# Kernel tuning notes

Hardware: AMD Instinct MI355X
Metric: run time of the kernel (lower is better)

The kernel has to match this reference:

```python
import jax, jax.numpy as jnp
import numpy as np

B, L, D, Z, H, N, G = 8, 2048, 1024, 128, 2048, 16, 32
MAXPOS = 2048
EPS = 1e-5
PRIOR_COUNT = 2.0  # TimestepNorm prior pseudo-count


def setup_inputs() -> dict:
    ks = jax.random.split(jax.random.key(0), 12)
    std = 0.02  # bert init
    return {
        "x": jax.random.normal(ks[0], (B, L, D), jnp.float32),
        "prior_mean": jnp.zeros((G,), jnp.float32),
        "prior_logv": jnp.zeros((G,), jnp.float32),
        "tn_weight": jnp.ones((D,), jnp.float32),
        "tn_bias": jnp.zeros((D,), jnp.float32),
        "delta": jax.random.normal(ks[1], (D, N), jnp.float32),
        "alpha": jax.random.normal(ks[2], (D, N), jnp.float32),
        "ema_beta": jax.random.normal(ks[3], (D, N), jnp.float32),
        "ema_gamma": jax.random.normal(ks[4], (D, N), jnp.float32),
        "omega": jax.random.normal(ks[5], (D,), jnp.float32),
        "rms_weight": jnp.ones((D,), jnp.float32),
        "Wv": jax.random.normal(ks[6], (H, D), jnp.float32) * std,
        "bv": jnp.zeros((H,), jnp.float32),
        "Wmx": jax.random.normal(ks[7], (Z + H + 2 * D, D), jnp.float32) * std,
        "bmx": jnp.zeros((Z + H + 2 * D,), jnp.float32),
        "Wh": jax.random.normal(ks[8], (D, H), jnp.float32) * std,
        "qk_gamma": jax.random.normal(ks[9], (2, Z), jnp.float32) * 0.1,
        "qk_beta": jax.random.normal(ks[10], (2, Z), jnp.float32) * 0.1,
        "rel_bias": jax.random.normal(ks[11], (2 * MAXPOS - 1,), jnp.float32) * 0.02,
    }


def timestep_norm(x, prior_mean, prior_logv, weight, bias):
    """Causal cumulative group norm with a prior (TimestepNorm)."""
    m = D // G  # features per group
    xg = x.reshape(B, L, G, m)
    s1 = jnp.cumsum(xg.sum(-1), axis=1)            # B,L,G  running sum
    s2 = jnp.cumsum((xg * xg).sum(-1), axis=1)     # B,L,G  running sum of squares
    cnt = PRIOR_COUNT + m * jnp.arange(1, L + 1, dtype=x.dtype)[None, :, None]
    pv = jnp.exp(prior_logv)
    mean = (PRIOR_COUNT * prior_mean + s1) / cnt
    var = (PRIOR_COUNT * (pv + prior_mean ** 2) + s2) / cnt - mean ** 2
    xn = (xg - mean[..., None]) * jax.lax.rsqrt(var[..., None] + EPS)
    return xn.reshape(B, L, D) * weight + bias


def multihead_ema(x, delta, alpha, ema_beta, ema_gamma, omega):
    """MultiHeadEMA: causal damped-EMA convolution via FFT, plus omega residual."""
    p = jax.nn.sigmoid(delta)                       # D,N
    a = jax.nn.sigmoid(alpha)
    q = 1.0 - p * a                                 # decay in (0,1)
    t = jnp.arange(L, dtype=x.dtype)
    vander = jnp.exp(t[None, None, :] * jnp.log(q)[:, :, None])  # D,N,L
    scale = 1.0 / jnp.sqrt(jnp.asarray(N, x.dtype))
    kern = jnp.einsum('dn,dnl,dn->dl', p * ema_beta, vander, ema_gamma * scale)
    xT = x.transpose(0, 2, 1)                       # B,D,L
    n = 2 * L
    out = jnp.fft.irfft(jnp.fft.rfft(xT, n=n) * jnp.fft.rfft(kern, n=n)[None], n=n)[..., :L]
    out = out + xT * omega[:, None]
    return out.transpose(0, 2, 1)


def _forward(x, prior_mean, prior_logv, tn_weight, tn_bias, delta, alpha,
             ema_beta, ema_gamma, omega, rms_weight, Wv, bv, Wmx, bmx, Wh,
             qk_gamma, qk_beta, rel_bias):
    residual = x
    xn = timestep_norm(x, prior_mean, prior_logv, tn_weight, tn_bias)
    v = jax.nn.silu(xn @ Wv.T + bv)                 # B,L,H
    mx = multihead_ema(xn, delta, alpha, ema_beta, ema_gamma, omega)
    mx = mx * jax.lax.rsqrt(jnp.mean(mx * mx, axis=-1, keepdims=True) + EPS) * rms_weight  # RMSNorm
    base = mx @ Wmx.T + bmx                         # B,L,Z+H+2D
    u = jax.nn.sigmoid(base[..., :D])
    zr = jax.nn.silu(base[..., D:D + Z + H])
    hx = base[..., D + Z + H:]
    z, r = zr[..., :Z], zr[..., Z:]
    zz = z[..., None, :] * qk_gamma + qk_beta       # B,L,2,Z
    q = zz[..., 0, :] * (Z ** -0.5)
    k = zz[..., 1, :]
    # simple relative positional bias: bias[i,j] = rel_bias[MAXPOS-1 + (j-i)]
    idx = (MAXPOS - 1) + (jnp.arange(L)[None, :] - jnp.arange(L)[:, None])
    qk = jnp.einsum('biz,bjz->bij', q, k) + rel_bias[idx]
    causal = jnp.tril(jnp.ones((L, L), bool))
    qk = jnp.where(causal, qk, -jnp.inf)
    attn = jax.nn.softmax(qk, axis=-1)              # B,L,L
    h = jnp.einsum('bij,bjh->bih', attn, v)         # B,L,H
    h = jax.nn.silu(hx + (h * r) @ Wh.T)            # B,L,D
    return residual + u * (h - residual)


def reference(x, prior_mean, prior_logv, tn_weight, tn_bias, delta, alpha,
              ema_beta, ema_gamma, omega, rms_weight, Wv, bv, Wmx, bmx, Wh,
              qk_gamma, qk_beta, rel_bias):
    return _forward(x, prior_mean, prior_logv, tn_weight, tn_bias, delta, alpha,
                    ema_beta, ema_gamma, omega, rms_weight, Wv, bv, Wmx, bmx, Wh,
                    qk_gamma, qk_beta, rel_bias)
```

## Files before the change

kernel.cpp:

```cpp
#include <hip/hip_runtime.h>
#include <stdint.h>

#define B_ 8
#define L_ 2048
#define D_ 1024
#define Z_ 128
#define H_ 2048
#define NE_ 16
#define G_ 32
#define MAXPOS_ 2048
#define NMX_ 4224
#define EPS_ 1e-5f
#define PC_ 2.0f
#define NTILE_ 16
#define NPACK_ 136
#define TILE_ELEMS_ 16384

typedef short bf16x8 __attribute__((ext_vector_type(8)));
typedef float f32x4 __attribute__((ext_vector_type(4)));

__device__ __forceinline__ float bf2f(uint16_t u) {
  union { uint32_t u; float f; } v; v.u = ((uint32_t)u) << 16; return v.f;
}
__device__ __forceinline__ uint16_t f2bf(float f) {
  union { float f; uint32_t u; } v; v.f = f;
  uint32_t r = (v.u + 0x7FFFu + ((v.u >> 16) & 1u)) >> 16;
  return (uint16_t)r;
}
__device__ __forceinline__ float sigmoidf_(float x) { return 1.f / (1.f + __expf(-x)); }
__device__ __forceinline__ float siluf_(float x) { return x / (1.f + __expf(-x)); }

__device__ __forceinline__ float waveRedSum(float v) {
  #pragma unroll
  for (int m = 32; m; m >>= 1) v += __shfl_xor(v, m, 64);
  return v;
}

__device__ __forceinline__ void gl2lds(const uint16_t* g, uint16_t* l) {
  __builtin_amdgcn_global_load_lds(
      (const __attribute__((address_space(1))) void*)g,
      (__attribute__((address_space(3))) void*)l, 16, 0, 0);
}

__global__ __launch_bounds__(256) void k_fallback(float* __restrict__ out, int n, float wsmb) {
  for (int i = blockIdx.x * 256 + threadIdx.x; i < n; i += gridDim.x * 256)
    out[i] = (i == 0) ? wsmb : 0.f;
}

__global__ __launch_bounds__(256) void k_f2bf(const float* __restrict__ src,
                                              uint16_t* __restrict__ dst, int n) {
  for (int i = blockIdx.x * 256 + threadIdx.x; i < n; i += gridDim.x * 256)
    dst[i] = f2bf(src[i]);
}

__global__ __launch_bounds__(256) void k_tnsum(const float* __restrict__ x,
                                               float* __restrict__ s1g,
                                               float* __restrict__ s2g) {
  const int bg = blockIdx.x;
  const int b = bg / G_, g = bg % G_;
  const int tid = threadIdx.x;
  const int j = tid & 31;
  const int lsub = tid >> 5;
  #pragma unroll
  for (int i = 0; i < 16; ++i) {
    const int l = blockIdx.y * 128 + i * 8 + lsub;
    float v = x[((size_t)(b * L_ + l)) * D_ + g * 32 + j];
    float a = v, sq = v * v;
    #pragma unroll
    for (int m = 1; m <= 16; m <<= 1) { a += __shfl_xor(a, m, 64); sq += __shfl_xor(sq, m, 64); }
    if (j == 0) { s1g[(size_t)bg * L_ + l] = a; s2g[(size_t)bg * L_ + l] = sq; }
  }
}

__global__ __launch_bounds__(64) void k_tnscan(float* __restrict__ s1g,
                                               float* __restrict__ s2g) {
  const int bg = blockIdx.x;
  const int lane = threadIdx.x;
  #pragma unroll
  for (int pass = 0; pass < 2; ++pass) {
    float* gp = (pass ? s2g : s1g) + (size_t)bg * L_;
    float loc[32];
    const int b0 = lane * 32;
    float tot = 0.f;
    #pragma unroll
    for (int t = 0; t < 32; ++t) { loc[t] = gp[b0 + t]; tot += loc[t]; }
    float incl = tot;
    #pragma unroll
    for (int off = 1; off < 64; off <<= 1) {
      float nv = __shfl_up(incl, off, 64);
      if (lane >= off) incl += nv;
    }
    float run = incl - tot;
    #pragma unroll
    for (int t = 0; t < 32; ++t) { run += loc[t]; gp[b0 + t] = run; }
  }
}

__global__ __launch_bounds__(256) void k_tnnorm(const float* __restrict__ x,
                                                const float* __restrict__ s1g,
                                                const float* __restrict__ s2g,
                                                const float* __restrict__ pm,
                                                const float* __restrict__ plv,
                                                const float* __restrict__ w,
                                                const float* __restrict__ bias,
                                                uint16_t* __restrict__ xn) {
  const int bg = blockIdx.x;
  const int b = bg / G_, g = bg % G_;
  const int tid = threadIdx.x;
  const int j = tid & 31;
  const int lsub = tid >> 5;
  const float pmv = pm[g];
  const float pvv = __expf(plv[g]);
  const float wj = w[g * 32 + j];
  const float bj = bias[g * 32 + j];
  const float pterm = PC_ * (pvv + pmv * pmv);
  #pragma unroll
  for (int i = 0; i < 16; ++i) {
    const int l = blockIdx.y * 128 + i * 8 + lsub;
    const size_t idx = ((size_t)(b * L_ + l)) * D_ + g * 32 + j;
    const float v = x[idx];
    const float cnt = PC_ + 32.f * (float)(l + 1);
    const float mean = (PC_ * pmv + s1g[(size_t)bg * L_ + l]) / cnt;
    const float var = (pterm + s2g[(size_t)bg * L_ + l]) / cnt - mean * mean;
    xn[idx] = f2bf((v - mean) * rsqrtf(var + EPS_) * wj + bj);
  }
}

__global__ __launch_bounds__(256) void k_tp16(const uint16_t* __restrict__ src,
                                              uint16_t* __restrict__ dst, int R, int C) {
  __shared__ uint16_t tile[64 * 65];
  const size_t batch = (size_t)R * C * blockIdx.z;
  const int c0 = blockIdx.x * 64, r0 = blockIdx.y * 64;
  const int t = threadIdx.x;
  const int rr = t >> 3;
  const int cc = (t & 7) * 8;
  #pragma unroll
  for (int p = 0; p < 2; ++p) {
    const int row = p * 32 + rr;
    bf16x8 v = *(const bf16x8*)&src[batch + (size_t)(r0 + row) * C + c0 + cc];
    #pragma unroll
    for (int i = 0; i < 8; ++i) tile[(cc + i) * 65 + row] = (uint16_t)v[i];
  }
  __syncthreads();
  #pragma unroll
  for (int p = 0; p < 2; ++p) {
    const int crow = p * 32 + rr;
    bf16x8 o;
    #pragma unroll
    for (int i = 0; i < 8; ++i) o[i] = (short)tile[crow * 65 + cc + i];
    *(bf16x8*)&dst[batch + (size_t)(c0 + crow) * R + r0 + cc] = o;
  }
}

__global__ __launch_bounds__(256) void k_tpf32(const float* __restrict__ src,
                                               float* __restrict__ dst, int R, int C) {
  __shared__ float tile[64 * 65];
  const size_t batch = (size_t)R * C * blockIdx.z;
  const int c0 = blockIdx.x * 64, r0 = blockIdx.y * 64;
  const int t = threadIdx.x;
  const int rr = t >> 4;
  const int cc = (t & 15) * 4;
  #pragma unroll
  for (int p = 0; p < 4; ++p) {
    const int row = p * 16 + rr;
    f32x4 v = *(const f32x4*)&src[batch + (size_t)(r0 + row) * C + c0 + cc];
    #pragma unroll
    for (int i = 0; i < 4; ++i) tile[(cc + i) * 65 + row] = v[i];
  }
  __syncthreads();
  #pragma unroll
  for (int p = 0; p < 4; ++p) {
    const int crow = p * 16 + rr;
    f32x4 o;
    #pragma unroll
    for (int i = 0; i < 4; ++i) o[i] = tile[crow * 65 + cc + i];
    *(f32x4*)&dst[batch + (size_t)(c0 + crow) * R + r0 + cc] = o;
  }
}

__global__ __launch_bounds__(64) void k_ema(const uint16_t* __restrict__ xnT,
                                            const float* __restrict__ delta,
                                            const float* __restrict__ alpha,
                                            const float* __restrict__ beta,
                                            const float* __restrict__ gamma,
                                            const float* __restrict__ omega,
                                            float* __restrict__ mxT) {
  __shared__ float hst[64 * NE_];
  const int bd = blockIdx.x;
  const int d = bd & (D_ - 1);
  const int c = threadIdx.x;

  float q[NE_], pb[NE_], gs[NE_];
  #pragma unroll
  for (int n = 0; n < NE_; ++n) {
    float p = sigmoidf_(delta[d * NE_ + n]);
    float a = sigmoidf_(alpha[d * NE_ + n]);
    q[n] = 1.f - p * a;
    pb[n] = p * beta[d * NE_ + n];
    gs[n] = gamma[d * NE_ + n] * 0.25f;
  }

  const uint16_t* xp = xnT + (size_t)bd * L_ + c * 32;
  bf16x8 xin[4];
  #pragma unroll
  for (int s = 0; s < 4; ++s) xin[s] = *(const bf16x8*)(xp + s * 8);

  float h[NE_];
  #pragma unroll
  for (int n = 0; n < NE_; ++n) h[n] = 0.f;

  #pragma unroll
  for (int k = 0; k < 32; ++k) {
    float xv = bf2f((uint16_t)xin[k >> 3][k & 7]);
    #pragma unroll
    for (int n = 0; n < NE_; ++n) h[n] = fmaf(q[n], h[n], pb[n] * xv);
  }
  #pragma unroll
  for (int n = 0; n < NE_; ++n) hst[c * NE_ + n] = h[n];
  __syncthreads();

  if (c < NE_) {
    float qq = q[c];
    float q32 = qq * qq; q32 *= q32; q32 *= q32; q32 *= q32; q32 *= q32;
    float hi = 0.f;
    for (int cc = 0; cc < 64; ++cc) {
      float cur = hst[cc * NE_ + c];
      hst[cc * NE_ + c] = hi;
      hi = fmaf(q32, hi, cur);
    }
  }
  __syncthreads();

  #pragma unroll
  for (int n = 0; n < NE_; ++n) h[n] = hst[c * NE_ + n];
  const float om = omega[d];
  float* op = mxT + (size_t)bd * L_ + c * 32;
  f32x4 ov;
  #pragma unroll
  for (int k = 0; k < 32; ++k) {
    float xv = bf2f((uint16_t)xin[k >> 3][k & 7]);
    float accv = 0.f;
    #pragma unroll
    for (int n = 0; n < NE_; ++n) {
      h[n] = fmaf(q[n], h[n], pb[n] * xv);
      accv = fmaf(gs[n], h[n], accv);
    }
    ov[k & 3] = accv + om * xv;
    if ((k & 3) == 3) *(f32x4*)(op + (k & ~3)) = ov;
  }
}

__global__ __launch_bounds__(256) void k_rms(const float* __restrict__ mx,
                                             const float* __restrict__ w,
                                             uint16_t* __restrict__ mxn) {
  __shared__ float red[4];
  const size_t row = blockIdx.x;
  const int tid = threadIdx.x;
  float ss = 0.f;
  #pragma unroll
  for (int i = 0; i < 4; ++i) {
    float v = mx[row * D_ + tid + i * 256];
    ss += v * v;
  }
  ss = waveRedSum(ss);
  if ((tid & 63) == 0) red[tid >> 6] = ss;
  __syncthreads();
  ss = red[0] + red[1] + red[2] + red[3];
  const float scale = rsqrtf(ss * (1.f / D_) + EPS_);
  #pragma unroll
  for (int i = 0; i < 4; ++i) {
    int dcol = tid + i * 256;
    mxn[row * D_ + dcol] = f2bf(mx[row * D_ + dcol] * scale * w[dcol]);
  }
}


template <int MODE>
__global__ __launch_bounds__(256, 4) void k_gemm128(
    const uint16_t* __restrict__ A, const uint16_t* __restrict__ Bm,
    int N, int K,
    const float* __restrict__ bias,
    float* __restrict__ outf, uint16_t* __restrict__ outb,
    uint16_t* __restrict__ ubuf,
    uint16_t* __restrict__ rbuf, float* __restrict__ hxbuf,
    const float* __restrict__ x0,
    const float* __restrict__ qkg, const float* __restrict__ qkb,
    uint16_t* __restrict__ qbuf, uint16_t* __restrict__ kbuf) {
  __shared__ uint16_t sm[17408];
  const int t = threadIdx.x;
  const int lane = t & 63, wave = t >> 6;
  const int quad = lane >> 4, r16 = lane & 15;
  const int wm = wave >> 1, wn = wave & 1;
  const int bm = blockIdx.x * 128;
  const int bn = blockIdx.y * 128;

  f32x4 acc[4][4];
  const f32x4 zf = {0.f, 0.f, 0.f, 0.f};
  #pragma unroll
  for (int i = 0; i < 4; ++i)
    #pragma unroll
    for (int j = 0; j < 4; ++j) acc[i][j] = zf;

  const int sgz = (((t & 3) ^ ((t >> 3) & 3)) << 3);
  const uint16_t* gA = A + (size_t)(bm + (t >> 2)) * K + sgz;
  const uint16_t* gB = Bm + (size_t)(bn + (t >> 2)) * K + sgz;
  const size_t qstep = (size_t)64 * K;
  uint16_t* lA = sm + t * 8;
  uint16_t* lB = sm + 4096 + t * 8;

  const int ga = ((quad ^ ((r16 >> 1) & 3)) << 3);
  const int aOff = (wm * 64 + r16) * 32 + ga;
  const int bOff = 4096 + (wn * 64 + r16) * 32 + ga;

#define STAGE(c, kb) do {                                                     \
    gl2lds(gA + (kb), lA + (c) * 8192);                                       \
    gl2lds(gA + qstep + (kb), lA + (c) * 8192 + 2048);                        \
    gl2lds(gB + (kb), lB + (c) * 8192);                                       \
    gl2lds(gB + qstep + (kb), lB + (c) * 8192 + 2048);                        \
  } while (0)

  const int NT = K >> 5;

  STAGE(0, 0);
  __syncthreads();

  bf16x8 af[4], bfr[4];
  for (int tt = 0; tt < NT; ++tt) {
    const int c = tt & 1;
    const int co = c * 8192;
    if (tt + 1 < NT) STAGE(c ^ 1, (tt + 1) * 32);
    #pragma unroll
    for (int j = 0; j < 4; ++j)
      bfr[j] = *(const bf16x8*)&sm[co + bOff + j * 512];
    #pragma unroll
    for (int i = 0; i < 4; ++i)
      af[i] = *(const bf16x8*)&sm[co + aOff + i * 512];
    #pragma unroll
    for (int i = 0; i < 4; ++i)
      #pragma unroll
      for (int j = 0; j < 4; ++j)
        acc[i][j] = __builtin_amdgcn_mfma_f32_16x16x32_bf16(
            af[i], bfr[j], acc[i][j], 0, 0, 0);
    __syncthreads();
  }
#undef STAGE

  if (MODE == 0) {
    #pragma unroll
    for (int i = 0; i < 4; ++i)
      #pragma unroll
      for (int j = 0; j < 4; ++j)
        #pragma unroll
        for (int r = 0; r < 4; ++r) {
          const int hloc = wn * 64 + j * 16 + r16;
          const int lloc = wm * 64 + i * 16 + quad * 4 + r;
          sm[hloc * 136 + lloc] = f2bf(siluf_(acc[i][j][r] + bias[bn + hloc]));
        }
    __syncthreads();
    const int bb = bm >> 11;
    const int lb = bm & 2047;
    uint16_t* vTb = outb + (size_t)bb * H_ * L_;
    #pragma unroll
    for (int p = 0; p < 8; ++p) {
      const int hloc = p * 16 + (t >> 4);
      const int l0 = (t & 15) * 8;
      bf16x8 v = *(const bf16x8*)&sm[hloc * 136 + l0];
      *(bf16x8*)&vTb[(size_t)(bn + hloc) * L_ + lb + l0] = v;
    }
  } else {
    #pragma unroll
    for (int i = 0; i < 4; ++i) {
      #pragma unroll
      for (int j = 0; j < 4; ++j) {
        #pragma unroll
        for (int r = 0; r < 4; ++r) {
          const int row = bm + wm * 64 + i * 16 + quad * 4 + r;
          const int col = bn + wn * 64 + j * 16 + r16;
          float val = acc[i][j][r];
          if (MODE == 1) {
            val += bias[col];
            if (col < D_) {
              ubuf[(size_t)row * D_ + col] = f2bf(sigmoidf_(val));
            } else if (col < D_ + Z_) {
              const int zc = col - D_;
              const float zv = siluf_(val);
              qbuf[(size_t)row * Z_ + zc] =
                  f2bf((zv * qkg[zc] + qkb[zc]) * 0.08838834764831845f);
              kbuf[(size_t)row * Z_ + zc] =
                  f2bf(zv * qkg[Z_ + zc] + qkb[Z_ + zc]);
            } else if (col < D_ + Z_ + H_) {
              rbuf[(size_t)row * H_ + (col - D_ - Z_)] = f2bf(siluf_(val));
            } else {
              hxbuf[(size_t)row * D_ + (col - D_ - Z_ - H_)] = val;
            }
          } else {
            const size_t idx = (size_t)row * N + col;
            float g = siluf_(val + hxbuf[idx]);
            float xv = x0[idx];
            outf[idx] = xv + bf2f(ubuf[idx]) * (g - xv);
          }
        }
      }
    }
  }
}

__global__ __launch_bounds__(256) void k_qksm(
    const uint16_t* __restrict__ qg, const uint16_t* __restrict__ kg,
    const float* __restrict__ relb, uint16_t* __restrict__ Pp) {
  __shared__ uint16_t Ks[2 * 16384];
  __shared__ float relwin[2 * 256];
  const int qt = blockIdx.x;
  const int bl = blockIdx.y;
  const int tid = threadIdx.x;
  const int w = tid >> 6, lane = tid & 63;
  const int quad = lane >> 4, r16 = lane & 15;
  const uint16_t* qb_b = qg + (size_t)bl * L_ * Z_;
  const uint16_t* kb_b = kg + (size_t)bl * L_ * Z_;
  uint16_t* P_b = Pp + (size_t)bl * NPACK_ * TILE_ELEMS_;

  const int ksg = (tid >> 4) * 128 + (((tid & 15) ^ ((tid >> 4) & 7)) << 3);
  const int kg7 = r16 & 7;

#define STGK(c, kt) do {                                                      \
    const uint16_t* src_ = kb_b + (size_t)(kt) * 128 * Z_;                    \
    _Pragma("unroll")                                                         \
    for (int s2 = 0; s2 < 8; ++s2)                                            \
      gl2lds(src_ + s2 * 2048 + ksg, Ks + (c) * 16384 + s2 * 2048 + tid * 8); \
    if (tid < 255)                                                            \
      relwin[(c) * 256 + tid] = relb[2047 + ((kt) - qt) * 128 - 127 + tid];   \
  } while (0)

  bf16x8 aq[2][4];
  #pragma unroll
  for (int i = 0; i < 2; ++i)
    #pragma unroll
    for (int s = 0; s < 4; ++s)
      aq[i][s] = *(const bf16x8*)&qb_b[(size_t)(qt * 128 + w * 32 + i * 16 + r16) * Z_ +
                                       s * 32 + quad * 8];

  float m8[8], l8[8];
  #pragma unroll
  for (int t = 0; t < 8; ++t) { m8[t] = -3.4e38f; l8[t] = 0.f; }

  const f32x4 zf = {0.f, 0.f, 0.f, 0.f};

  STGK(0, 0);
  __syncthreads();
  for (int kt = 0; kt <= qt; ++kt) {
    const int cur = kt & 1;
    if (kt < qt) STGK(cur ^ 1, kt + 1);
    const uint16_t* Kc = Ks + cur * 16384;
    const float* rw = relwin + cur * 256;
    #pragma unroll
    for (int j = 0; j < 8; ++j) {
      f32x4 a0 = zf, a1 = zf;
      #pragma unroll
      for (int s = 0; s < 4; ++s) {
        bf16x8 bk = *(const bf16x8*)&Kc[(j * 16 + r16) * 128 +
                                        (((s * 4 + quad) ^ kg7) << 3)];
        a0 = __builtin_amdgcn_mfma_f32_16x16x32_bf16(aq[0][s], bk, a0, 0, 0, 0);
        a1 = __builtin_amdgcn_mfma_f32_16x16x32_bf16(aq[1][s], bk, a1, 0, 0, 0);
      }
      #pragma unroll
      for (int i = 0; i < 2; ++i) {
        const f32x4 av = i ? a1 : a0;
        #pragma unroll
        for (int r = 0; r < 4; ++r) {
          const int rloc = w * 32 + i * 16 + quad * 4 + r;
          const int cloc = j * 16 + r16;
          if (kt < qt || cloc <= rloc) {
            const float v = av[r] + rw[cloc - rloc + 127];
            const int t = i * 4 + r;
            const float mn = fmaxf(m8[t], v);
            l8[t] = l8[t] * __expf(m8[t] - mn) + __expf(v - mn);
            m8[t] = mn;
          }
        }
      }
    }
    __syncthreads();
  }

  #pragma unroll
  for (int t = 0; t < 8; ++t) {
    #pragma unroll
    for (int msk = 1; msk <= 8; msk <<= 1) {
      const float mo = __shfl_xor(m8[t], msk, 64);
      const float lo = __shfl_xor(l8[t], msk, 64);
      const float mn = fmaxf(m8[t], mo);
      l8[t] = l8[t] * __expf(m8[t] - mn) + lo * __expf(mo - mn);
      m8[t] = mn;
    }
    l8[t] = 1.f / l8[t];
  }

  STGK(0, 0);
  __syncthreads();
  for (int kt = 0; kt <= qt; ++kt) {
    const int cur = kt & 1;
    if (kt < qt) STGK(cur ^ 1, kt + 1);
    const uint16_t* Kc = Ks + cur * 16384;
    const float* rw = relwin + cur * 256;
    uint16_t* Pt = P_b + (size_t)(qt * (qt + 1) / 2 + kt) * TILE_ELEMS_;
    #pragma unroll
    for (int j = 0; j < 8; ++j) {
      f32x4 a0 = zf, a1 = zf;
      #pragma unroll
      for (int s = 0; s < 4; ++s) {
        bf16x8 bk = *(const bf16x8*)&Kc[(j * 16 + r16) * 128 +
                                        (((s * 4 + quad) ^ kg7) << 3)];
        a0 = __builtin_amdgcn_mfma_f32_16x16x32_bf16(aq[0][s], bk, a0, 0, 0, 0);
        a1 = __builtin_amdgcn_mfma_f32_16x16x32_bf16(aq[1][s], bk, a1, 0, 0, 0);
      }
      #pragma unroll
      for (int i = 0; i < 2; ++i) {
        const f32x4 av = i ? a1 : a0;
        #pragma unroll
        for (int r = 0; r < 4; ++r) {
          const int rloc = w * 32 + i * 16 + quad * 4 + r;
          const int cloc = j * 16 + r16;
          const int t = i * 4 + r;
          float p = 0.f;
          if (kt < qt || cloc <= rloc) {
            const float v = av[r] + rw[cloc - rloc + 127];
            p = __expf(v - m8[t]) * l8[t];
          }
          Pt[rloc * 128 + cloc] = f2bf(p);
        }
      }
    }
    __syncthreads();
  }
#undef STGK
}

__global__ __launch_bounds__(512, 4) void k_pv(
    const uint16_t* __restrict__ Pp, const uint16_t* __restrict__ vT,
    uint16_t* __restrict__ rh) {
  __shared__ uint16_t sm[24576];
  const int qt = NTILE_ - 1 - blockIdx.x;
  const int bn = blockIdx.y * 256;
  const int bl = blockIdx.z;
  const uint16_t* Pq = Pp + (size_t)bl * NPACK_ * TILE_ELEMS_ +
                       (size_t)(qt * (qt + 1) / 2) * TILE_ELEMS_;
  const uint16_t* v_b = vT + (size_t)bl * H_ * L_;
  uint16_t* rh_b = rh + (size_t)bl * L_ * H_;

  const int tid = threadIdx.x;
  const int wave = tid >> 6, lane = tid & 63;
  const int quad = lane >> 4, r16 = lane & 15;
  const int wm = wave >> 2, wn = wave & 3;
  const int rowW = wm * 64, colW = wn * 64;

  f32x4 acc[4][4];
  const f32x4 zf = {0.f, 0.f, 0.f, 0.f};
  #pragma unroll
  for (int i = 0; i < 4; ++i)
    #pragma unroll
    for (int j = 0; j < 4; ++j) acc[i][j] = zf;

  const int rA = tid >> 2;
  const int sg = (((tid & 3) ^ ((tid >> 3) & 3)) << 3);
  const int gpv = ((quad ^ ((r16 >> 1) & 3)) << 3);

#define PVSTAGE(c, s) do {                                                    \
    const int kt_ = (s) >> 2, ks_ = (s) & 3;                                  \
    gl2lds(Pq + (size_t)kt_ * TILE_ELEMS_ + rA * 128 + ks_ * 32 + sg,         \
           sm + (c) * 12288 + tid * 8);                                       \
    const uint16_t* Bt_ = v_b + (size_t)(bn + rA) * L_ + kt_ * 128 +          \
                          ks_ * 32 + sg;                                      \
    gl2lds(Bt_, sm + (c) * 12288 + 4096 + tid * 8);                           \
    gl2lds(Bt_ + (size_t)128 * L_, sm + (c) * 12288 + 8192 + tid * 8);        \
  } while (0)

  const int S = 4 * (qt + 1);

  PVSTAGE(0, 0);
  __syncthreads();

  bf16x8 af[4], bfr[4];
  for (int s = 0; s < S; ++s) {
    const int c = s & 1;
    const int co = c * 12288;
    if (s + 1 < S) PVSTAGE(c ^ 1, s + 1);
    #pragma unroll
    for (int j = 0; j < 4; ++j)
      bfr[j] = *(const bf16x8*)&sm[co + 4096 + (colW + j * 16 + r16) * 32 + gpv];
    #pragma unroll
    for (int i = 0; i < 4; ++i)
      af[i] = *(const bf16x8*)&sm[co + (rowW + i * 16 + r16) * 32 + gpv];
    #pragma unroll
    for (int i = 0; i < 4; ++i)
      #pragma unroll
      for (int j = 0; j < 4; ++j)
        acc[i][j] = __builtin_amdgcn_mfma_f32_16x16x32_bf16(af[i], bfr[j], acc[i][j], 0, 0, 0);
    __syncthreads();
  }
#undef PVSTAGE

  #pragma unroll
  for (int i = 0; i < 4; ++i) {
    #pragma unroll
    for (int j = 0; j < 4; ++j) {
      #pragma unroll
      for (int r = 0; r < 4; ++r) {
        const int row = qt * 128 + rowW + i * 16 + quad * 4 + r;
        const int col = bn + colW + j * 16 + r16;
        const size_t idx = (size_t)row * H_ + col;
        const float rv = bf2f(rh_b[idx]);
        rh_b[idx] = f2bf(acc[i][j][r] * rv);
      }
    }
  }
}

extern "C" void kernel_launch(void* const* d_in, const int* in_sizes, int n_in,
                              void* d_out, int out_size, void* d_ws, size_t ws_size,
                              hipStream_t stream) {
  (void)in_sizes; (void)n_in;
  const float* x         = (const float*)d_in[0];
  const float* prior_mean= (const float*)d_in[1];
  const float* prior_logv= (const float*)d_in[2];
  const float* tn_w      = (const float*)d_in[3];
  const float* tn_b      = (const float*)d_in[4];
  const float* delta     = (const float*)d_in[5];
  const float* alpha     = (const float*)d_in[6];
  const float* ema_beta  = (const float*)d_in[7];
  const float* ema_gamma = (const float*)d_in[8];
  const float* omega     = (const float*)d_in[9];
  const float* rms_w     = (const float*)d_in[10];
  const float* Wv        = (const float*)d_in[11];
  const float* bv        = (const float*)d_in[12];
  const float* Wmx       = (const float*)d_in[13];
  const float* bmx       = (const float*)d_in[14];
  const float* Wh        = (const float*)d_in[15];
  const float* qk_gamma  = (const float*)d_in[16];
  const float* qk_beta   = (const float*)d_in[17];
  const float* rel_bias  = (const float*)d_in[18];
  float* out = (float*)d_out;

  const int BL = B_ * L_;
  const size_t MB = 1024 * 1024;
  const size_t REQUIRED = 256 * MB;

  if (ws_size < REQUIRED) {
    k_fallback<<<dim3(4096), dim3(256), 0, stream>>>(out, out_size, (float)(ws_size / MB));
    return;
  }

  char* p = (char*)d_ws;
  uint16_t* xn   = (uint16_t*)(p);
  uint16_t* ubuf = (uint16_t*)(p);
  float*    s1g  = (float*)   (p + 32 * MB);
  float*    s2g  = (float*)   (p + 34 * MB);
  uint16_t* xnT  = (uint16_t*)(p + 32 * MB);
  uint16_t* mxn  = (uint16_t*)(p + 32 * MB);
  uint16_t* vT   = (uint16_t*)(p + 64 * MB);
  uint16_t* wv_b = (uint16_t*)(p + 128 * MB);
  float*    mx   = (float*)   (p + 128 * MB);
  uint16_t* rbuf = (uint16_t*)(p + 128 * MB);
  uint16_t* wmx_b = (uint16_t*)(p + 192 * MB);
  uint16_t* wh_b  = (uint16_t*)(p + 192 * MB);
  uint16_t* qb    = (uint16_t*)(p + 209 * MB);
  uint16_t* kb2   = (uint16_t*)(p + 213 * MB);
  uint16_t* Ppack = (uint16_t*)(p + 217 * MB);
  float* mxT = out;
  float* hx  = out;

  k_f2bf<<<dim3(1024), dim3(256), 0, stream>>>(Wv, wv_b, H_ * D_);
  k_f2bf<<<dim3(2048), dim3(256), 0, stream>>>(Wmx, wmx_b, NMX_ * D_);
  k_tnsum<<<dim3(B_ * G_, 16), dim3(256), 0, stream>>>(x, s1g, s2g);
  k_tnscan<<<dim3(B_ * G_), dim3(64), 0, stream>>>(s1g, s2g);
  k_tnnorm<<<dim3(B_ * G_, 16), dim3(256), 0, stream>>>(
      x, s1g, s2g, prior_mean, prior_logv, tn_w, tn_b, xn);
  k_tp16<<<dim3(D_ / 64, L_ / 64, B_), dim3(256), 0, stream>>>(xn, xnT, L_, D_);
  k_gemm128<0><<<dim3(BL / 128, H_ / 128), dim3(256), 0, stream>>>(
      xn, wv_b, H_, D_, bv, nullptr, vT,
      nullptr, nullptr, nullptr, nullptr, nullptr, nullptr, nullptr, nullptr);
  k_ema<<<dim3(B_ * D_), dim3(64), 0, stream>>>(xnT, delta, alpha, ema_beta, ema_gamma, omega, mxT);
  k_tpf32<<<dim3(L_ / 64, D_ / 64, B_), dim3(256), 0, stream>>>(mxT, mx, D_, L_);
  k_rms<<<dim3(BL), dim3(256), 0, stream>>>(mx, rms_w, mxn);
  k_gemm128<1><<<dim3(BL / 128, NMX_ / 128), dim3(256), 0, stream>>>(
      mxn, wmx_b, NMX_, D_, bmx, nullptr, nullptr,
      ubuf, rbuf, hx, nullptr, qk_gamma, qk_beta, qb, kb2);
  k_qksm<<<dim3(NTILE_, B_), dim3(256), 0, stream>>>(qb, kb2, rel_bias, Ppack);
  k_pv<<<dim3(NTILE_, H_ / 256, B_), dim3(512), 0, stream>>>(Ppack, vT, rbuf);
  k_f2bf<<<dim3(1024), dim3(256), 0, stream>>>(Wh, wh_b, D_ * H_);
  k_gemm128<4><<<dim3(BL / 128, D_ / 128), dim3(256), 0, stream>>>(
      rbuf, wh_b, D_, H_, nullptr, out, nullptr,
      ubuf, nullptr, hx, x, nullptr, nullptr, nullptr, nullptr);
}
```

Baseline: 1.153 ms.

## Fuse xn transpose into timestep norm and stage GEMM epilogue stores via LDS

The timestep-norm kernel now also writes the transposed bf16 activations through a shared-memory tile, so the separate transpose kernel and its extra read of xn are removed. The s1/s2 scratch buffers are moved so they do not overlap xnT. The mixed-projection GEMM epilogue is split per column tile: u, r, q and k outputs are staged in LDS and written with vectorized 16-byte stores instead of scattered 2-byte stores, and hx is written directly. This adds extra barriers and LDS traffic in the epilogue.

```diff
diff --git a/kernel.cpp b/kernel.cpp
--- a/kernel.cpp
+++ b/kernel.cpp
@@ -103,7 +103,9 @@
                                                 const float* __restrict__ plv,
                                                 const float* __restrict__ w,
                                                 const float* __restrict__ bias,
-                                                uint16_t* __restrict__ xn) {
+                                                uint16_t* __restrict__ xn,
+                                                uint16_t* __restrict__ xnT) {
+  __shared__ uint16_t xt[32 * 136];
   const int bg = blockIdx.x;
   const int b = bg / G_, g = bg % G_;
   const int tid = threadIdx.x;
@@ -122,34 +124,15 @@
     const float cnt = PC_ + 32.f * (float)(l + 1);
     const float mean = (PC_ * pmv + s1g[(size_t)bg * L_ + l]) / cnt;
     const float var = (pterm + s2g[(size_t)bg * L_ + l]) / cnt - mean * mean;
-    xn[idx] = f2bf((v - mean) * rsqrtf(var + EPS_) * wj + bj);
-  }
-}
-
-__global__ __launch_bounds__(256) void k_tp16(const uint16_t* __restrict__ src,
-                                              uint16_t* __restrict__ dst, int R, int C) {
-  __shared__ uint16_t tile[64 * 65];
-  const size_t batch = (size_t)R * C * blockIdx.z;
-  const int c0 = blockIdx.x * 64, r0 = blockIdx.y * 64;
-  const int t = threadIdx.x;
-  const int rr = t >> 3;
-  const int cc = (t & 7) * 8;
-  #pragma unroll
-  for (int p = 0; p < 2; ++p) {
-    const int row = p * 32 + rr;
-    bf16x8 v = *(const bf16x8*)&src[batch + (size_t)(r0 + row) * C + c0 + cc];
-    #pragma unroll
-    for (int i = 0; i < 8; ++i) tile[(cc + i) * 65 + row] = (uint16_t)v[i];
-  }
-  __syncthreads();
-  #pragma unroll
-  for (int p = 0; p < 2; ++p) {
-    const int crow = p * 32 + rr;
-    bf16x8 o;
-    #pragma unroll
-    for (int i = 0; i < 8; ++i) o[i] = (short)tile[crow * 65 + cc + i];
-    *(bf16x8*)&dst[batch + (size_t)(c0 + crow) * R + r0 + cc] = o;
-  }
+    const uint16_t o = f2bf((v - mean) * rsqrtf(var + EPS_) * wj + bj);
+    xn[idx] = o;
+    xt[j * 136 + i * 8 + lsub] = o;
+  }
+  __syncthreads();
+  const int row = tid >> 3, ch = tid & 7;
+  uint16_t* dst = xnT + ((size_t)(b * D_ + g * 32 + row)) * L_ + blockIdx.y * 128 + ch * 16;
+  *(bf16x8*)&dst[0] = *(const bf16x8*)&xt[row * 136 + ch * 16];
+  *(bf16x8*)&dst[8] = *(const bf16x8*)&xt[row * 136 + ch * 16 + 8];
 }
 
 __global__ __launch_bounds__(256) void k_tpf32(const float* __restrict__ src,
@@ -367,6 +350,72 @@
       bf16x8 v = *(const bf16x8*)&sm[hloc * 136 + l0];
       *(bf16x8*)&vTb[(size_t)(bn + hloc) * L_ + lb + l0] = v;
     }
+  } else if (MODE == 1) {
+    const int rt = bn >> 7;
+    if (rt >= 25) {
+      #pragma unroll
+      for (int i = 0; i < 4; ++i)
+        #pragma unroll
+        for (int j = 0; j < 4; ++j)
+          #pragma unroll
+          for (int r = 0; r < 4; ++r) {
+            const int row = bm + wm * 64 + i * 16 + quad * 4 + r;
+            const int col = bn + wn * 64 + j * 16 + r16;
+            hxbuf[(size_t)row * D_ + (col - D_ - Z_ - H_)] = acc[i][j][r] + bias[col];
+          }
+    } else if (rt == 8) {
+      #pragma unroll
+      for (int pass = 0; pass < 2; ++pass) {
+        #pragma unroll
+        for (int i = 0; i < 4; ++i)
+          #pragma unroll
+          for (int j = 0; j < 4; ++j)
+            #pragma unroll
+            for (int r = 0; r < 4; ++r) {
+              const int rowloc = wm * 64 + i * 16 + quad * 4 + r;
+              const int zc = wn * 64 + j * 16 + r16;
+              const float zv = siluf_(acc[i][j][r] + bias[D_ + zc]);
+              const float o = pass == 0
+                  ? (zv * qkg[zc] + qkb[zc]) * 0.08838834764831845f
+                  : zv * qkg[Z_ + zc] + qkb[Z_ + zc];
+              sm[rowloc * 136 + zc] = f2bf(o);
+            }
+        __syncthreads();
+        uint16_t* dstb = pass == 0 ? qbuf : kbuf;
+        #pragma unroll
+        for (int p = 0; p < 8; ++p) {
+          const int row = p * 16 + (t >> 4);
+          const int c0 = (t & 15) * 8;
+          bf16x8 v = *(const bf16x8*)&sm[row * 136 + c0];
+          *(bf16x8*)&dstb[(size_t)(bm + row) * Z_ + c0] = v;
+        }
+        __syncthreads();
+      }
+    } else {
+      const bool isU = rt < 8;
+      #pragma unroll
+      for (int i = 0; i < 4; ++i)
+        #pragma unroll
+        for (int j = 0; j < 4; ++j)
+          #pragma unroll
+          for (int r = 0; r < 4; ++r) {
+            const int rowloc = wm * 64 + i * 16 + quad * 4 + r;
+            const int colloc = wn * 64 + j * 16 + r16;
+            const float val = acc[i][j][r] + bias[bn + colloc];
+            sm[rowloc * 136 + colloc] = f2bf(isU ? sigmoidf_(val) : siluf_(val));
+          }
+      __syncthreads();
+      #pragma unroll
+      for (int p = 0; p < 8; ++p) {
+        const int row = p * 16 + (t >> 4);
+        const int c0 = (t & 15) * 8;
+        bf16x8 v = *(const bf16x8*)&sm[row * 136 + c0];
+        if (isU)
+          *(bf16x8*)&ubuf[(size_t)(bm + row) * D_ + bn + c0] = v;
+        else
+          *(bf16x8*)&rbuf[(size_t)(bm + row) * H_ + (bn - D_ - Z_) + c0] = v;
+      }
+    }
   } else {
     #pragma unroll
     for (int i = 0; i < 4; ++i) {
@@ -376,29 +425,10 @@
         for (int r = 0; r < 4; ++r) {
           const int row = bm + wm * 64 + i * 16 + quad * 4 + r;
           const int col = bn + wn * 64 + j * 16 + r16;
-          float val = acc[i][j][r];
-          if (MODE == 1) {
-            val += bias[col];
-            if (col < D_) {
-              ubuf[(size_t)row * D_ + col] = f2bf(sigmoidf_(val));
-            } else if (col < D_ + Z_) {
-              const int zc = col - D_;
-              const float zv = siluf_(val);
-              qbuf[(size_t)row * Z_ + zc] =
-                  f2bf((zv * qkg[zc] + qkb[zc]) * 0.08838834764831845f);
-              kbuf[(size_t)row * Z_ + zc] =
-                  f2bf(zv * qkg[Z_ + zc] + qkb[Z_ + zc]);
-            } else if (col < D_ + Z_ + H_) {
-              rbuf[(size_t)row * H_ + (col - D_ - Z_)] = f2bf(siluf_(val));
-            } else {
-              hxbuf[(size_t)row * D_ + (col - D_ - Z_ - H_)] = val;
-            }
-          } else {
-            const size_t idx = (size_t)row * N + col;
-            float g = siluf_(val + hxbuf[idx]);
-            float xv = x0[idx];
-            outf[idx] = xv + bf2f(ubuf[idx]) * (g - xv);
-          }
+          const size_t idx = (size_t)row * N + col;
+          float g = siluf_(acc[i][j][r] + hxbuf[idx]);
+          float xv = x0[idx];
+          outf[idx] = xv + bf2f(ubuf[idx]) * (g - xv);
         }
       }
     }
@@ -652,12 +682,12 @@
   char* p = (char*)d_ws;
   uint16_t* xn   = (uint16_t*)(p);
   uint16_t* ubuf = (uint16_t*)(p);
-  float*    s1g  = (float*)   (p + 32 * MB);
-  float*    s2g  = (float*)   (p + 34 * MB);
   uint16_t* xnT  = (uint16_t*)(p + 32 * MB);
   uint16_t* mxn  = (uint16_t*)(p + 32 * MB);
   uint16_t* vT   = (uint16_t*)(p + 64 * MB);
   uint16_t* wv_b = (uint16_t*)(p + 128 * MB);
+  float*    s1g  = (float*)   (p + 132 * MB);
+  float*    s2g  = (float*)   (p + 134 * MB);
   float*    mx   = (float*)   (p + 128 * MB);
   uint16_t* rbuf = (uint16_t*)(p + 128 * MB);
   uint16_t* wmx_b = (uint16_t*)(p + 192 * MB);
@@ -673,8 +703,7 @@
   k_tnsum<<<dim3(B_ * G_, 16), dim3(256), 0, stream>>>(x, s1g, s2g);
   k_tnscan<<<dim3(B_ * G_), dim3(64), 0, stream>>>(s1g, s2g);
   k_tnnorm<<<dim3(B_ * G_, 16), dim3(256), 0, stream>>>(
-      x, s1g, s2g, prior_mean, prior_logv, tn_w, tn_b, xn);
-  k_tp16<<<dim3(D_ / 64, L_ / 64, B_), dim3(256), 0, stream>>>(xn, xnT, L_, D_);
+      x, s1g, s2g, prior_mean, prior_logv, tn_w, tn_b, xn, xnT);
   k_gemm128<0><<<dim3(BL / 128, H_ / 128), dim3(256), 0, stream>>>(
       xn, wv_b, H_, D_, bv, nullptr, vT,
       nullptr, nullptr, nullptr, nullptr, nullptr, nullptr, nullptr, nullptr);
```

New measurement: 1.109 ms. 1.04x faster.
